# Performance work log

Measured on AMD Instinct MI355X. Metric: run time of the kernel, lower is better.

The kernel has to match this reference:

```python
import jax, jax.numpy as jnp
import numpy as np

N_NODES = 50000
N_EDGES = 1600000
IN_F = 256
OUT_F = 128
N_REL = 500
NEG_SLOPE = 0.2
EPS = 1e-10


def setup_inputs() -> dict:
    key = jax.random.key(0)
    ks = jax.random.split(key, 7)
    h = jax.random.normal(ks[0], (N_NODES, IN_F), dtype=jnp.float32)
    rows = jax.random.randint(ks[1], (N_EDGES,), 0, N_NODES)
    cols = jax.random.randint(ks[2], (N_EDGES,), 0, N_NODES)
    edge_types = jax.random.randint(ks[3], (N_EDGES,), 0, N_REL)
    # learned params (xavier-ish small scale)
    W = jax.random.normal(ks[4], (IN_F, OUT_F), dtype=jnp.float32) * 0.05
    rel_emb = jax.random.normal(ks[5], (N_REL, OUT_F), dtype=jnp.float32) * 0.05
    a = jax.random.normal(ks[6], (2 * OUT_F + OUT_F,), dtype=jnp.float32) * 0.05
    return {"h": h, "rows": rows, "cols": cols, "edge_types": edge_types,
            "W": W, "rel_emb": rel_emb, "a": a}


def reference(h, rows, cols, edge_types, W, rel_emb, a):
    N = h.shape[0]
    d = W.shape[1]
    Wh = h @ W                                   # [N, out]
    # a^T [Wh_i || Wh_j || r] decomposed to avoid materializing the concat
    a_i, a_j, a_r = a[:d], a[d:2 * d], a[2 * d:]
    s_node_i = Wh @ a_i                          # [N]
    s_node_j = Wh @ a_j                          # [N]
    s_rel = rel_emb @ a_r                        # [R]
    e = s_node_i[rows] + s_node_j[cols] + s_rel[edge_types]   # [E]
    e = jax.nn.leaky_relu(e, negative_slope=NEG_SLOPE)
    e = e - jnp.max(e)                           # global max-shift as in original
    exp_e = jnp.exp(e)
    sum_exp = jax.ops.segment_sum(exp_e, rows, num_segments=N)  # [N]
    alpha = exp_e / (sum_exp[rows] + EPS)        # [E]  (dropout is identity in eval)
    # sparse matmul: h'_i = sum_{j in N(i)} alpha_ij * Wh_j
    h_prime = jax.ops.segment_sum(alpha[:, None] * Wh[cols], rows, num_segments=N)
    return jax.nn.elu(h_prime)
```

## Files before the change

kernel.cpp:

```cpp
#include <hip/hip_runtime.h>

#define N_NODES 50000
#define N_EDGES 1600000
#define IN_F    256
#define OUT_F   128
#define N_REL   500
#define NEG_SLOPE 0.2f
#define EPS_F   1e-10f
#define GEMM_ROWS 64

#define NB       3125
#define CAP      768
#define BIN_CHUNK 4096
#define NBIN_BLK 391

typedef __attribute__((ext_vector_type(8))) __bf16 bf16x8;
typedef __attribute__((ext_vector_type(4))) float f32x4;
typedef __attribute__((ext_vector_type(2))) float f32x2;

static __device__ __forceinline__ float bf2f(unsigned short u) {
    unsigned v = ((unsigned)u) << 16;
    float f;
    __builtin_memcpy(&f, &v, 4);
    return f;
}
static __device__ __forceinline__ unsigned short f2bf(float f) {
    unsigned u;
    __builtin_memcpy(&u, &f, 4);
    unsigned rounding = 0x7fffu + ((u >> 16) & 1u);
    u += rounding;
    return (unsigned short)(u >> 16);
}

__global__ __launch_bounds__(256) void wconv_k(
    const float* __restrict__ W,
    const float* __restrict__ a,
    unsigned short* __restrict__ WbfT,
    unsigned short* __restrict__ wai_bf, unsigned short* __restrict__ waj_bf)
{
    int wid  = threadIdx.x >> 6;
    int lane = threadIdx.x & 63;
    int k    = blockIdx.x * 4 + wid;
    int n0   = lane * 2;
    float2 wv2 = *(const float2*)(W + (size_t)k * OUT_F + n0);
    WbfT[(size_t)n0 * IN_F + k]       = f2bf(wv2.x);
    WbfT[(size_t)(n0 + 1) * IN_F + k] = f2bf(wv2.y);
    float si = wv2.x * a[n0] + wv2.y * a[n0 + 1];
    float sj = wv2.x * a[OUT_F + n0] + wv2.y * a[OUT_F + n0 + 1];
    #pragma unroll
    for (int off = 32; off; off >>= 1) {
        si += __shfl_xor(si, off, 64);
        sj += __shfl_xor(sj, off, 64);
    }
    if (lane == 0) { wai_bf[k] = f2bf(si); waj_bf[k] = f2bf(sj); }
}

__global__ __launch_bounds__(256) void srel_k(
    const float* __restrict__ rel_emb,
    const float* __restrict__ a,
    float* __restrict__ s_rel)
{
    int rid  = blockIdx.x * 4 + (threadIdx.x >> 6);
    int lane = threadIdx.x & 63;
    if (rid >= N_REL) return;
    float2 re = *(const float2*)(rel_emb + (size_t)rid * OUT_F + 2 * lane);
    float2 ar = *(const float2*)(a + 2 * OUT_F + 2 * lane);
    float sr = re.x * ar.x + re.y * ar.y;
    #pragma unroll
    for (int off = 32; off; off >>= 1) sr += __shfl_xor(sr, off, 64);
    if (lane == 0) s_rel[rid] = sr;
}

__global__ __launch_bounds__(256) void gemm_wh(
    const float* __restrict__ h,
    const unsigned short* __restrict__ WbfT,
    const unsigned short* __restrict__ wai_bf, const unsigned short* __restrict__ waj_bf,
    unsigned short* __restrict__ Whb,
    float* __restrict__ s_i, float* __restrict__ s_j)
{
    const int t    = threadIdx.x;
    const int wv   = t >> 6;
    const int lane = t & 63;
    const int quad = lane >> 4;
    const int l15  = lane & 15;
    const int r0   = blockIdx.x * GEMM_ROWS;

    bf16x8 Bfrag[2][8];
    #pragma unroll
    for (int ct2 = 0; ct2 < 2; ++ct2) {
        int n = 32 * wv + 16 * ct2 + l15;
        #pragma unroll
        for (int ks = 0; ks < 8; ++ks)
            Bfrag[ct2][ks] = *(const bf16x8*)(WbfT + (size_t)n * IN_F + 32 * ks + 8 * quad);
    }
    bf16x8 Sfrag[8];
    if (wv == 0) {
        const unsigned short* ssrc = (l15 == 0) ? wai_bf : waj_bf;
        #pragma unroll
        for (int ks = 0; ks < 8; ++ks) {
            if (l15 < 2) Sfrag[ks] = *(const bf16x8*)(ssrc + 32 * ks + 8 * quad);
            else         Sfrag[ks] = (bf16x8)(__bf16)0.0f;
        }
    }

    #pragma unroll 1
    for (int rg = 0; rg < 4; ++rg) {
        int row = r0 + rg * 16 + l15;
        if (row > N_NODES - 1) row = N_NODES - 1;
        const float* hp = h + (size_t)row * IN_F + quad * 8;
        bf16x8 Afrag[8];
        #pragma unroll
        for (int ks = 0; ks < 8; ++ks) {
            float4 u0 = *(const float4*)(hp + ks * 32);
            float4 u1 = *(const float4*)(hp + ks * 32 + 4);
            bf16x8 af;
            af[0] = (__bf16)u0.x; af[1] = (__bf16)u0.y; af[2] = (__bf16)u0.z; af[3] = (__bf16)u0.w;
            af[4] = (__bf16)u1.x; af[5] = (__bf16)u1.y; af[6] = (__bf16)u1.z; af[7] = (__bf16)u1.w;
            Afrag[ks] = af;
        }
        f32x4 acc0 = {0.f, 0.f, 0.f, 0.f};
        f32x4 acc1 = {0.f, 0.f, 0.f, 0.f};
        #pragma unroll
        for (int ks = 0; ks < 8; ++ks) {
            acc0 = __builtin_amdgcn_mfma_f32_16x16x32_bf16(Afrag[ks], Bfrag[0][ks], acc0, 0, 0, 0);
            acc1 = __builtin_amdgcn_mfma_f32_16x16x32_bf16(Afrag[ks], Bfrag[1][ks], acc1, 0, 0, 0);
        }
        #pragma unroll
        for (int reg = 0; reg < 4; ++reg) {
            int gr = r0 + 16 * rg + quad * 4 + reg;
            if (gr < N_NODES) {
                Whb[(size_t)gr * OUT_F + 32 * wv + l15]      = f2bf(acc0[reg]);
                Whb[(size_t)gr * OUT_F + 32 * wv + 16 + l15] = f2bf(acc1[reg]);
            }
        }
        if (wv == 0) {
            f32x4 acc2 = {0.f, 0.f, 0.f, 0.f};
            #pragma unroll
            for (int ks = 0; ks < 8; ++ks)
                acc2 = __builtin_amdgcn_mfma_f32_16x16x32_bf16(Afrag[ks], Sfrag[ks], acc2, 0, 0, 0);
            #pragma unroll
            for (int reg = 0; reg < 4; ++reg) {
                int gr = r0 + 16 * rg + quad * 4 + reg;
                if (gr < N_NODES) {
                    if (l15 == 0) s_i[gr] = acc2[reg];
                    else if (l15 == 1) s_j[gr] = acc2[reg];
                }
            }
        }
    }
}

__global__ __launch_bounds__(256) void bin_k(
    const int* __restrict__ rows, const int* __restrict__ cols, const int* __restrict__ types,
    const float* __restrict__ s_i, const float* __restrict__ s_j, const float* __restrict__ s_rel,
    int* __restrict__ cnt, uint2* __restrict__ epk)
{
    __shared__ int hist[NB];
    __shared__ int lbase[NB];
    __shared__ int cur[NB];
    __shared__ float srl[N_REL];
    int t = threadIdx.x;
    for (int i = t; i < NB; i += 256) { hist[i] = 0; cur[i] = 0; }
    for (int i = t; i < N_REL; i += 256) srl[i] = s_rel[i];
    __syncthreads();

    int base = blockIdx.x * BIN_CHUNK;
    float cw[16];
    unsigned cm[16];
    #pragma unroll
    for (int i = 0; i < 16; ++i) {
        int e = base + t + 256 * i;
        if (e < N_EDGES) {
            int r = rows[e], c = cols[e], ty = types[e];
            float v = s_i[r] + s_j[c] + srl[ty];
            v = (v > 0.f) ? v : NEG_SLOPE * v;
            cw[i] = __expf(v);
            int b = r >> 4;
            cm[i] = (unsigned)c | ((unsigned)(r & 15) << 16) | ((unsigned)b << 20);
            atomicAdd(&hist[b], 1);
        } else {
            cw[i] = 0.f;
            cm[i] = 0xffffffffu;
        }
    }
    __syncthreads();
    for (int i = t; i < NB; i += 256)
        if (hist[i] > 0) lbase[i] = atomicAdd(&cnt[i], hist[i]);
    __syncthreads();
    #pragma unroll
    for (int i = 0; i < 16; ++i) {
        int e = base + t + 256 * i;
        if (e < N_EDGES) {
            int b = cm[i] >> 20;
            int loc = lbase[b] + atomicAdd(&cur[b], 1);
            if (loc < CAP)
                epk[(size_t)b * CAP + loc] = make_uint2(__float_as_uint(cw[i]), cm[i] & 0xfffffu);
        }
    }
}

__global__ __launch_bounds__(256, 8) void bucket_agg(
    const int* __restrict__ cnt, const uint2* __restrict__ epk,
    const unsigned short* __restrict__ Whb,
    float* __restrict__ out)
{
    __shared__ uint2 sorted[CAP];
    __shared__ int hist[16];
    __shared__ int offs[17];
    __shared__ int cur[16];

    const int t    = threadIdx.x;
    const int wid  = t >> 6;
    const int lane = t & 63;
    const int b    = blockIdx.x;
    const int n    = min(cnt[b], CAP);
    const uint2* ep = epk + (size_t)b * CAP;

    if (t < 16) hist[t] = 0;
    __syncthreads();

    uint2 rec[3];
    #pragma unroll
    for (int i = 0; i < 3; ++i) {
        int idx = t + 256 * i;
        rec[i] = (idx < n) ? ep[idx] : make_uint2(0u, 0xffffffffu);
    }
    #pragma unroll
    for (int i = 0; i < 3; ++i)
        if (rec[i].y != 0xffffffffu) atomicAdd(&hist[(rec[i].y >> 16) & 15], 1);
    __syncthreads();
    if (wid == 0 && lane < 16) {
        int v = hist[lane];
        #pragma unroll
        for (int off = 1; off < 16; off <<= 1) {
            int u = __shfl_up(v, off, 64);
            if (lane >= off) v += u;
        }
        offs[lane + 1] = v;
        if (lane == 0) offs[0] = 0;
        cur[lane] = v - hist[lane];
    }
    __syncthreads();
    #pragma unroll
    for (int i = 0; i < 3; ++i) {
        if (rec[i].y != 0xffffffffu) {
            int pos = atomicAdd(&cur[(rec[i].y >> 16) & 15], 1);
            sorted[pos] = make_uint2(rec[i].x, (rec[i].y & 0xffffu) << 8);
        }
    }
    __syncthreads();

    const unsigned hh = lane >> 5;
    const unsigned lb = (unsigned)(lane & 31) << 3;
    const char* wbase = (const char*)Whb;

    #pragma unroll 1
    for (int rl = 0; rl < 4; ++rl) {
        const int row = wid * 4 + rl;
        int i = offs[row];
        const int e1 = offs[row + 1];
        f32x2 a01 = {0.f, 0.f};
        f32x2 a23 = {0.f, 0.f};
        float s = 0.f;

        for (; i + 12 <= e1; i += 12) {
            uint2 rc[6];
            #pragma unroll
            for (int j = 0; j < 6; ++j) rc[j] = sorted[i + 2 * j + hh];
            uint2 pk[6];
            #pragma unroll
            for (int j = 0; j < 6; ++j)
                pk[j] = *(const uint2*)(wbase + (rc[j].y + lb));
            #pragma unroll
            for (int j = 0; j < 6; ++j) {
                float w = __uint_as_float(rc[j].x);
                unsigned p0 = pk[j].x, p1 = pk[j].y;
                a01.x = __builtin_fmaf(__uint_as_float(p0 << 16),          w, a01.x);
                a01.y = __builtin_fmaf(__uint_as_float(p0 & 0xffff0000u),  w, a01.y);
                a23.x = __builtin_fmaf(__uint_as_float(p1 << 16),          w, a23.x);
                a23.y = __builtin_fmaf(__uint_as_float(p1 & 0xffff0000u),  w, a23.y);
                s += w;
            }
        }
        for (; i + 4 <= e1; i += 4) {
            uint2 rc0 = sorted[i + hh];
            uint2 rc1 = sorted[i + 2 + hh];
            uint2 pk0 = *(const uint2*)(wbase + (rc0.y + lb));
            uint2 pk1 = *(const uint2*)(wbase + (rc1.y + lb));
            float w0 = __uint_as_float(rc0.x);
            float w1 = __uint_as_float(rc1.x);
            a01.x = __builtin_fmaf(__uint_as_float(pk0.x << 16),         w0, a01.x);
            a01.y = __builtin_fmaf(__uint_as_float(pk0.x & 0xffff0000u), w0, a01.y);
            a23.x = __builtin_fmaf(__uint_as_float(pk0.y << 16),         w0, a23.x);
            a23.y = __builtin_fmaf(__uint_as_float(pk0.y & 0xffff0000u), w0, a23.y);
            a01.x = __builtin_fmaf(__uint_as_float(pk1.x << 16),         w1, a01.x);
            a01.y = __builtin_fmaf(__uint_as_float(pk1.x & 0xffff0000u), w1, a01.y);
            a23.x = __builtin_fmaf(__uint_as_float(pk1.y << 16),         w1, a23.x);
            a23.y = __builtin_fmaf(__uint_as_float(pk1.y & 0xffff0000u), w1, a23.y);
            s += w0 + w1;
        }
        for (; i < e1; i += 2) {
            int idx = i + (int)hh;
            uint2 r0 = (idx < e1) ? sorted[idx] : make_uint2(0u, 0u);
            uint2 pk0 = *(const uint2*)(wbase + (r0.y + lb));
            float w = __uint_as_float(r0.x);
            a01.x = __builtin_fmaf(__uint_as_float(pk0.x << 16),         w, a01.x);
            a01.y = __builtin_fmaf(__uint_as_float(pk0.x & 0xffff0000u), w, a01.y);
            a23.x = __builtin_fmaf(__uint_as_float(pk0.y << 16),         w, a23.x);
            a23.y = __builtin_fmaf(__uint_as_float(pk0.y & 0xffff0000u), w, a23.y);
            s += w;
        }

        s     += __shfl_xor(s, 32, 64);
        a01.x += __shfl_xor(a01.x, 32, 64);
        a01.y += __shfl_xor(a01.y, 32, 64);
        a23.x += __shfl_xor(a23.x, 32, 64);
        a23.y += __shfl_xor(a23.y, 32, 64);

        if (hh == 0) {
            const int grow = b * 16 + row;
            float inv = 1.f / (s + EPS_F);
            float v0 = a01.x * inv, v1 = a01.y * inv;
            float v2 = a23.x * inv, v3 = a23.y * inv;
            v0 = (v0 > 0.f) ? v0 : (__expf(v0) - 1.f);
            v1 = (v1 > 0.f) ? v1 : (__expf(v1) - 1.f);
            v2 = (v2 > 0.f) ? v2 : (__expf(v2) - 1.f);
            v3 = (v3 > 0.f) ? v3 : (__expf(v3) - 1.f);
            *(float4*)(out + (size_t)grow * OUT_F + ((lane & 31) << 2)) =
                make_float4(v0, v1, v2, v3);
        }
    }
}

extern "C" void kernel_launch(void* const* d_in, const int* in_sizes, int n_in,
                              void* d_out, int out_size, void* d_ws, size_t ws_size,
                              hipStream_t stream)
{
    const float* h     = (const float*)d_in[0];
    const int*   rows  = (const int*)d_in[1];
    const int*   cols  = (const int*)d_in[2];
    const int*   types = (const int*)d_in[3];
    const float* W     = (const float*)d_in[4];
    const float* rel   = (const float*)d_in[5];
    const float* a     = (const float*)d_in[6];

    char* ws = (char*)d_ws;
    size_t off = 0;
    auto alloc = [&](size_t bytes) -> void* {
        void* p = ws + off;
        off = (off + bytes + 255) & ~(size_t)255;
        return p;
    };
    unsigned short* Whb   = (unsigned short*)alloc((size_t)N_NODES * OUT_F * 2);
    unsigned short* WbfT  = (unsigned short*)alloc((size_t)IN_F * OUT_F * 2);
    unsigned short* wai_bf = (unsigned short*)alloc((size_t)IN_F * 2);
    unsigned short* waj_bf = (unsigned short*)alloc((size_t)IN_F * 2);
    float* s_i    = (float*)alloc((size_t)N_NODES * 4);
    float* s_j    = (float*)alloc((size_t)N_NODES * 4);
    float* s_rel  = (float*)alloc((size_t)N_REL * 4);
    int*   cnt    = (int*)alloc((size_t)NB * 4);
    uint2* epk    = (uint2*)alloc((size_t)NB * CAP * 8);
    (void)ws_size; (void)in_sizes; (void)n_in; (void)out_size;

    hipMemsetAsync(cnt, 0, (size_t)NB * 4, stream);

    wconv_k<<<64, 256, 0, stream>>>(W, a, WbfT, wai_bf, waj_bf);
    srel_k<<<(N_REL + 3) / 4, 256, 0, stream>>>(rel, a, s_rel);
    gemm_wh<<<(N_NODES + GEMM_ROWS - 1) / GEMM_ROWS, 256, 0, stream>>>(
        h, WbfT, wai_bf, waj_bf, Whb, s_i, s_j);
    bin_k<<<NBIN_BLK, 256, 0, stream>>>(rows, cols, types, s_i, s_j, s_rel, cnt, epk);
    bucket_agg<<<NB, 256, 0, stream>>>(cnt, epk, Whb, (float*)d_out);
}
```

Baseline: 239.2 us.

## Replace block-local binning with per-edge global atomics; unroll aggregation gather to 8

The binning kernel drops its shared-memory histogram, block-level base reservation and second scatter pass. Instead, each thread handles one edge and claims a bucket slot with a global atomicAdd on the per-bucket counter. This removes three large shared arrays and two syncs, but sends about 1.6M global atomics to 3125 counters, so contention goes up. The aggregation inner loop now issues 8 gather loads per batch instead of 6, with a sched_barrier to keep the loads grouped ahead of the FMAs, for more memory-level parallelism at some register cost.

```diff
diff --git a/kernel.cpp b/kernel.cpp
--- a/kernel.cpp
+++ b/kernel.cpp
@@ -11,8 +11,6 @@
 
 #define NB       3125
 #define CAP      768
-#define BIN_CHUNK 4096
-#define NBIN_BLK 391
 
 typedef __attribute__((ext_vector_type(8))) __bf16 bf16x8;
 typedef __attribute__((ext_vector_type(4))) float f32x4;
@@ -155,48 +153,17 @@
     const float* __restrict__ s_i, const float* __restrict__ s_j, const float* __restrict__ s_rel,
     int* __restrict__ cnt, uint2* __restrict__ epk)
 {
-    __shared__ int hist[NB];
-    __shared__ int lbase[NB];
-    __shared__ int cur[NB];
-    __shared__ float srl[N_REL];
-    int t = threadIdx.x;
-    for (int i = t; i < NB; i += 256) { hist[i] = 0; cur[i] = 0; }
-    for (int i = t; i < N_REL; i += 256) srl[i] = s_rel[i];
-    __syncthreads();
-
-    int base = blockIdx.x * BIN_CHUNK;
-    float cw[16];
-    unsigned cm[16];
-    #pragma unroll
-    for (int i = 0; i < 16; ++i) {
-        int e = base + t + 256 * i;
-        if (e < N_EDGES) {
-            int r = rows[e], c = cols[e], ty = types[e];
-            float v = s_i[r] + s_j[c] + srl[ty];
-            v = (v > 0.f) ? v : NEG_SLOPE * v;
-            cw[i] = __expf(v);
-            int b = r >> 4;
-            cm[i] = (unsigned)c | ((unsigned)(r & 15) << 16) | ((unsigned)b << 20);
-            atomicAdd(&hist[b], 1);
-        } else {
-            cw[i] = 0.f;
-            cm[i] = 0xffffffffu;
-        }
-    }
-    __syncthreads();
-    for (int i = t; i < NB; i += 256)
-        if (hist[i] > 0) lbase[i] = atomicAdd(&cnt[i], hist[i]);
-    __syncthreads();
-    #pragma unroll
-    for (int i = 0; i < 16; ++i) {
-        int e = base + t + 256 * i;
-        if (e < N_EDGES) {
-            int b = cm[i] >> 20;
-            int loc = lbase[b] + atomicAdd(&cur[b], 1);
-            if (loc < CAP)
-                epk[(size_t)b * CAP + loc] = make_uint2(__float_as_uint(cw[i]), cm[i] & 0xfffffu);
-        }
-    }
+    int e = blockIdx.x * 256 + threadIdx.x;
+    if (e >= N_EDGES) return;
+    int r = rows[e], c = cols[e], ty = types[e];
+    float v = s_i[r] + s_j[c] + s_rel[ty];
+    v = (v > 0.f) ? v : NEG_SLOPE * v;
+    float w = __expf(v);
+    int b = r >> 4;
+    int loc = atomicAdd(&cnt[b], 1);
+    if (loc < CAP)
+        epk[(size_t)b * CAP + loc] =
+            make_uint2(__float_as_uint(w), ((unsigned)(r & 15) << 16) | (unsigned)c);
 }
 
 __global__ __launch_bounds__(256, 8) void bucket_agg(
@@ -263,16 +230,17 @@
         f32x2 a23 = {0.f, 0.f};
         float s = 0.f;
 
-        for (; i + 12 <= e1; i += 12) {
-            uint2 rc[6];
-            #pragma unroll
-            for (int j = 0; j < 6; ++j) rc[j] = sorted[i + 2 * j + hh];
-            uint2 pk[6];
-            #pragma unroll
-            for (int j = 0; j < 6; ++j)
+        for (; i + 16 <= e1; i += 16) {
+            uint2 rc[8];
+            #pragma unroll
+            for (int j = 0; j < 8; ++j) rc[j] = sorted[i + 2 * j + hh];
+            uint2 pk[8];
+            #pragma unroll
+            for (int j = 0; j < 8; ++j)
                 pk[j] = *(const uint2*)(wbase + (rc[j].y + lb));
-            #pragma unroll
-            for (int j = 0; j < 6; ++j) {
+            __builtin_amdgcn_sched_barrier(0);
+            #pragma unroll
+            for (int j = 0; j < 8; ++j) {
                 float w = __uint_as_float(rc[j].x);
                 unsigned p0 = pk[j].x, p1 = pk[j].y;
                 a01.x = __builtin_fmaf(__uint_as_float(p0 << 16),          w, a01.x);
@@ -368,6 +336,6 @@
     srel_k<<<(N_REL + 3) / 4, 256, 0, stream>>>(rel, a, s_rel);
     gemm_wh<<<(N_NODES + GEMM_ROWS - 1) / GEMM_ROWS, 256, 0, stream>>>(
         h, WbfT, wai_bf, waj_bf, Whb, s_i, s_j);
-    bin_k<<<NBIN_BLK, 256, 0, stream>>>(rows, cols, types, s_i, s_j, s_rel, cnt, epk);
+    bin_k<<<N_EDGES / 256, 256, 0, stream>>>(rows, cols, types, s_i, s_j, s_rel, cnt, epk);
     bucket_agg<<<NB, 256, 0, stream>>>(cnt, epk, Whb, (float*)d_out);
 }
```

Measured after the change: 335.6 us. +40.3%, slower.

## Merge prep kernels with counter zeroing, pad bin counters, halve bin chunk

Applied to the files above, without the earlier changes.

The weight conversion, relation-score and memset launches are merged into one prep kernel that also zeroes the bucket counters, removing two launches and a memset. Bucket counters are padded to 64-byte stride so global atomics from different blocks on neighbouring buckets no longer share a cache line. The binning kernel processes 2048 edges per block over twice as many blocks, and it drops the separate cursor array by decrementing the histogram to get local slots, which cuts shared memory. The trade is more global atomics, since each block now adds per-bucket counts for half as many edges, plus a larger counter array.

```diff
diff --git a/kernel.cpp b/kernel.cpp
--- a/kernel.cpp
+++ b/kernel.cpp
@@ -11,8 +11,9 @@
 
 #define NB       3125
 #define CAP      768
-#define BIN_CHUNK 4096
-#define NBIN_BLK 391
+#define BIN_CHUNK 2048
+#define NBIN_BLK 782
+#define PREP_BLK 189
 
 typedef __attribute__((ext_vector_type(8))) __bf16 bf16x8;
 typedef __attribute__((ext_vector_type(4))) float f32x4;
@@ -32,43 +33,44 @@
     return (unsigned short)(u >> 16);
 }
 
-__global__ __launch_bounds__(256) void wconv_k(
+__global__ __launch_bounds__(256) void prep_k(
     const float* __restrict__ W,
     const float* __restrict__ a,
+    const float* __restrict__ rel_emb,
     unsigned short* __restrict__ WbfT,
-    unsigned short* __restrict__ wai_bf, unsigned short* __restrict__ waj_bf)
-{
+    unsigned short* __restrict__ wai_bf, unsigned short* __restrict__ waj_bf,
+    float* __restrict__ s_rel,
+    int* __restrict__ cnt)
+{
+    for (int i = blockIdx.x * 256 + threadIdx.x; i < NB; i += PREP_BLK * 256)
+        cnt[i << 4] = 0;
+
     int wid  = threadIdx.x >> 6;
     int lane = threadIdx.x & 63;
-    int k    = blockIdx.x * 4 + wid;
-    int n0   = lane * 2;
-    float2 wv2 = *(const float2*)(W + (size_t)k * OUT_F + n0);
-    WbfT[(size_t)n0 * IN_F + k]       = f2bf(wv2.x);
-    WbfT[(size_t)(n0 + 1) * IN_F + k] = f2bf(wv2.y);
-    float si = wv2.x * a[n0] + wv2.y * a[n0 + 1];
-    float sj = wv2.x * a[OUT_F + n0] + wv2.y * a[OUT_F + n0 + 1];
-    #pragma unroll
-    for (int off = 32; off; off >>= 1) {
-        si += __shfl_xor(si, off, 64);
-        sj += __shfl_xor(sj, off, 64);
-    }
-    if (lane == 0) { wai_bf[k] = f2bf(si); waj_bf[k] = f2bf(sj); }
-}
-
-__global__ __launch_bounds__(256) void srel_k(
-    const float* __restrict__ rel_emb,
-    const float* __restrict__ a,
-    float* __restrict__ s_rel)
-{
-    int rid  = blockIdx.x * 4 + (threadIdx.x >> 6);
-    int lane = threadIdx.x & 63;
-    if (rid >= N_REL) return;
-    float2 re = *(const float2*)(rel_emb + (size_t)rid * OUT_F + 2 * lane);
-    float2 ar = *(const float2*)(a + 2 * OUT_F + 2 * lane);
-    float sr = re.x * ar.x + re.y * ar.y;
-    #pragma unroll
-    for (int off = 32; off; off >>= 1) sr += __shfl_xor(sr, off, 64);
-    if (lane == 0) s_rel[rid] = sr;
+    if (blockIdx.x < 64) {
+        int k    = blockIdx.x * 4 + wid;
+        int n0   = lane * 2;
+        float2 wv2 = *(const float2*)(W + (size_t)k * OUT_F + n0);
+        WbfT[(size_t)n0 * IN_F + k]       = f2bf(wv2.x);
+        WbfT[(size_t)(n0 + 1) * IN_F + k] = f2bf(wv2.y);
+        float si = wv2.x * a[n0] + wv2.y * a[n0 + 1];
+        float sj = wv2.x * a[OUT_F + n0] + wv2.y * a[OUT_F + n0 + 1];
+        #pragma unroll
+        for (int off = 32; off; off >>= 1) {
+            si += __shfl_xor(si, off, 64);
+            sj += __shfl_xor(sj, off, 64);
+        }
+        if (lane == 0) { wai_bf[k] = f2bf(si); waj_bf[k] = f2bf(sj); }
+    } else {
+        int rid = (blockIdx.x - 64) * 4 + wid;
+        if (rid >= N_REL) return;
+        float2 re = *(const float2*)(rel_emb + (size_t)rid * OUT_F + 2 * lane);
+        float2 ar = *(const float2*)(a + 2 * OUT_F + 2 * lane);
+        float sr = re.x * ar.x + re.y * ar.y;
+        #pragma unroll
+        for (int off = 32; off; off >>= 1) sr += __shfl_xor(sr, off, 64);
+        if (lane == 0) s_rel[rid] = sr;
+    }
 }
 
 __global__ __launch_bounds__(256) void gemm_wh(
@@ -157,18 +159,17 @@
 {
     __shared__ int hist[NB];
     __shared__ int lbase[NB];
-    __shared__ int cur[NB];
     __shared__ float srl[N_REL];
     int t = threadIdx.x;
-    for (int i = t; i < NB; i += 256) { hist[i] = 0; cur[i] = 0; }
+    for (int i = t; i < NB; i += 256) hist[i] = 0;
     for (int i = t; i < N_REL; i += 256) srl[i] = s_rel[i];
     __syncthreads();
 
     int base = blockIdx.x * BIN_CHUNK;
-    float cw[16];
-    unsigned cm[16];
-    #pragma unroll
-    for (int i = 0; i < 16; ++i) {
+    float cw[8];
+    unsigned cm[8];
+    #pragma unroll
+    for (int i = 0; i < 8; ++i) {
         int e = base + t + 256 * i;
         if (e < N_EDGES) {
             int r = rows[e], c = cols[e], ty = types[e];
@@ -185,14 +186,13 @@
     }
     __syncthreads();
     for (int i = t; i < NB; i += 256)
-        if (hist[i] > 0) lbase[i] = atomicAdd(&cnt[i], hist[i]);
-    __syncthreads();
-    #pragma unroll
-    for (int i = 0; i < 16; ++i) {
-        int e = base + t + 256 * i;
-        if (e < N_EDGES) {
+        if (hist[i] > 0) lbase[i] = atomicAdd(&cnt[i << 4], hist[i]);
+    __syncthreads();
+    #pragma unroll
+    for (int i = 0; i < 8; ++i) {
+        if (cm[i] != 0xffffffffu) {
             int b = cm[i] >> 20;
-            int loc = lbase[b] + atomicAdd(&cur[b], 1);
+            int loc = lbase[b] + atomicSub(&hist[b], 1) - 1;
             if (loc < CAP)
                 epk[(size_t)b * CAP + loc] = make_uint2(__float_as_uint(cw[i]), cm[i] & 0xfffffu);
         }
@@ -213,7 +213,7 @@
     const int wid  = t >> 6;
     const int lane = t & 63;
     const int b    = blockIdx.x;
-    const int n    = min(cnt[b], CAP);
+    const int n    = min(cnt[b << 4], CAP);
     const uint2* ep = epk + (size_t)b * CAP;
 
     if (t < 16) hist[t] = 0;
@@ -358,14 +358,11 @@
     float* s_i    = (float*)alloc((size_t)N_NODES * 4);
     float* s_j    = (float*)alloc((size_t)N_NODES * 4);
     float* s_rel  = (float*)alloc((size_t)N_REL * 4);
-    int*   cnt    = (int*)alloc((size_t)NB * 4);
+    int*   cnt    = (int*)alloc((size_t)NB * 16 * 4);
     uint2* epk    = (uint2*)alloc((size_t)NB * CAP * 8);
     (void)ws_size; (void)in_sizes; (void)n_in; (void)out_size;
 
-    hipMemsetAsync(cnt, 0, (size_t)NB * 4, stream);
-
-    wconv_k<<<64, 256, 0, stream>>>(W, a, WbfT, wai_bf, waj_bf);
-    srel_k<<<(N_REL + 3) / 4, 256, 0, stream>>>(rel, a, s_rel);
+    prep_k<<<PREP_BLK, 256, 0, stream>>>(W, a, rel, WbfT, wai_bf, waj_bf, s_rel, cnt);
     gemm_wh<<<(N_NODES + GEMM_ROWS - 1) / GEMM_ROWS, 256, 0, stream>>>(
         h, WbfT, wai_bf, waj_bf, Whb, s_i, s_j);
     bin_k<<<NBIN_BLK, 256, 0, stream>>>(rows, cols, types, s_i, s_j, s_rel, cnt, epk);
```

After: 273.8 us. 14.4% more time.
